# Kernel optimization log

Measured on AMD Instinct MI355X. Metric: run time of the kernel, lower is better.

Reference implementation:

```python
import jax, jax.numpy as jnp
import numpy as np
from jax import lax

WIN = 11
SIGMA = 1.5
C1 = 0.01 ** 2
C2 = 0.03 ** 2


def _gauss_window(c):
    x = np.arange(WIN) - WIN // 2
    g = np.exp(-(x ** 2) / (2.0 * SIGMA ** 2))
    g = g / g.sum()
    w2d = np.outer(g, g).astype(np.float32)  # [11,11]
    return jnp.asarray(np.broadcast_to(w2d, (c, 1, WIN, WIN)).copy())


def _dwconv(x, kernel, groups):
    # x: [B,C,H,W], kernel: [C,1,kh,kw] depthwise, stride 1, SAME padding
    return lax.conv_general_dilated(
        x, kernel, window_strides=(1, 1), padding='SAME',
        dimension_numbers=('NCHW', 'OIHW', 'NCHW'),
        feature_group_count=groups)


_SOBEL_X = jnp.asarray(np.array([[-1, 0, 1], [-2, 0, 2], [-1, 0, 1]], np.float32))
_SOBEL_Y = jnp.asarray(np.array([[1, 2, 1], [0, 0, 0], [-1, -2, -1]], np.float32))


def _sobel_xy(x):
    # x: [B,3,H,W] -> depthwise 3x3 sobel on each channel (same as per-channel conv2d)
    c = x.shape[1]
    kx = jnp.broadcast_to(_SOBEL_X, (c, 1, 3, 3))
    ky = jnp.broadcast_to(_SOBEL_Y, (c, 1, 3, 3))
    return _dwconv(x, kx, c), _dwconv(x, ky, c)


def _rgb2ycrcb(im):
    R, G, B = im[:, 0:1], im[:, 1:2], im[:, 2:3]
    Y = 0.299 * R + 0.587 * G + 0.114 * B
    Cr = (R - Y) * 0.713 + 0.5
    Cb = (B - Y) * 0.564 + 0.5
    return Y, Cr, Cb


def _ssim(img1, img2, channel):
    w = _gauss_window(channel)
    mu1 = _dwconv(img1, w, channel)
    mu2 = _dwconv(img2, w, channel)
    mu1_sq = mu1 * mu1
    mu2_sq = mu2 * mu2
    mu12 = mu1 * mu2
    s1 = _dwconv(img1 * img1, w, channel) - mu1_sq
    s2 = _dwconv(img2 * img2, w, channel) - mu2_sq
    s12 = _dwconv(img1 * img2, w, channel) - mu12
    ssim_map = ((2 * mu12 + C1) * (2 * s12 + C2)) / ((mu1_sq + mu2_sq + C1) * (s1 + s2 + C2))
    return ssim_map.mean()


def _l1(a, b):
    return jnp.mean(jnp.abs(a - b))


def setup_inputs() -> dict:
    key = jax.random.key(0)
    k1, k2, k3 = jax.random.split(key, 3)
    shp = (16, 3, 512, 512)
    return {
        'input_vis': jax.random.uniform(k1, shp, jnp.float32),
        'input_ir': jax.random.uniform(k2, shp, jnp.float32),
        'fuse': jax.random.uniform(k3, shp, jnp.float32),
    }


def reference(input_vis, input_ir, fuse):
    # color components
    _, Cr_F, Cb_F = _rgb2ycrcb(fuse)
    _, Cr_V, Cb_V = _rgb2ycrcb(input_vis)
    Y_ir = input_ir[:, 0:1]

    # sobel gradients (depthwise over 3 channels == per-channel conv + cat)
    Fgx, Fgy = _sobel_xy(fuse)
    Vgx, Vgy = _sobel_xy(input_vis)
    Igx, Igy = _sobel_xy(input_ir)
    joint_gx = jnp.maximum(Vgx, Igx)
    joint_gy = jnp.maximum(Vgy, Igy)
    joint_int = jnp.maximum(input_vis, input_ir)

    con_loss = _l1(fuse, joint_int)
    gradient_loss = 0.5 * _l1(Fgx, joint_gx) + 0.5 * _l1(Fgy, joint_gy)
    color_loss = _l1(Cb_F, Cb_V) + _l1(Cr_F, Cr_V)

    # SSIM: rgb-vs-fused (3ch) and ir-Y vs gray(fused) (1ch)
    ssim_rgb = _ssim(input_vis, fuse, 3)
    gray_fused = (0.2989 * fuse[:, 0:1] + 0.587 * fuse[:, 1:2] + 0.114 * fuse[:, 2:3])
    ssim_ir = _ssim(Y_ir, gray_fused, 1)
    ssim_loss = 1.0 - (ssim_rgb + ssim_ir) / 2.0

    return 0.5 * con_loss + 0.2 * gradient_loss + 1.0 * color_loss + 0.1 * ssim_loss
```

## Files before the change

kernel.cpp:

```cpp
#include <hip/hip_runtime.h>

#define IMG_H 512
#define IMG_W 512
#define CH_STRIDE (IMG_H*IMG_W)
#define IMG_STRIDE (3*CH_STRIDE)

using f4 = __attribute__((ext_vector_type(4))) float;
using h2 = __attribute__((ext_vector_type(2))) _Float16;
using h4 = __attribute__((ext_vector_type(4))) _Float16;
using h8 = __attribute__((ext_vector_type(8))) _Float16;

#define NSLOT 64
#define SLOT_F 32

__global__ __launch_bounds__(256) void k_zero(float* __restrict__ acc) {
  int i = threadIdx.x;
  *(f4*)&acc[i*8]     = f4{0,0,0,0};
  *(f4*)&acc[i*8 + 4] = f4{0,0,0,0};
}

__device__ __forceinline__ float block_sum(float v, float* red) {
  #pragma unroll
  for (int o = 32; o > 0; o >>= 1) v += __shfl_down(v, o, 64);
  __syncthreads();
  if ((threadIdx.x & 63) == 0) red[threadIdx.x >> 6] = v;
  __syncthreads();
  return red[0] + red[1] + red[2] + red[3];
}

__device__ __forceinline__ h8 splat8(_Float16 v) { return h8{v,v,v,v,v,v,v,v}; }

#define R1W 68
#define R1N (18*R1W)

#define SXW 80
#define SXH 26
#define HB8 264
#define SSIM_SX_B (SXH*SXW*2)
#define SSIM_HB_B (SXH*HB8*2)
#define SMEM_BYTES (2*SSIM_SX_B + SSIM_HB_B)

#define N_SSIM 16384

__global__ __launch_bounds__(256, 7) void k_main(
    const float* __restrict__ vis, const float* __restrict__ ir,
    const float* __restrict__ fuse, float* __restrict__ acc)
{
  __shared__ __align__(16) char smem[SMEM_BYTES];
  __shared__ float red[4];
  const int tid = threadIdx.x;
  const int bid = blockIdx.x;
  float* aslot = acc + (bid & (NSLOT-1))*SLOT_F;

  if (bid < N_SSIM) {
    const int z = bid >> 8;
    const int n = z >> 2, pair = z & 3;
    const int x0 = (bid & 7)*64;
    const int y0 = ((bid >> 3) & 31)*16;
    _Float16* sx = (_Float16*)smem;
    _Float16* sy = (_Float16*)(smem + SSIM_SX_B);
    _Float16* hb = (_Float16*)(smem + 2*SSIM_SX_B);

    _Float16 gh[11];
    h2 gh2[11];
    {
      const float gu[6] = {0.00386592014f, 0.02856550078f, 0.13533528324f,
                           0.41111229050f, 0.80073740292f, 1.0f};
      float g[11], gs = 0.f;
      #pragma unroll
      for (int i = 0; i < 11; ++i) { g[i] = gu[i < 6 ? i : 10 - i]; gs += g[i]; }
      #pragma unroll
      for (int i = 0; i < 11; ++i) {
        g[i] /= gs;
        gh[i] = (_Float16)g[i];
        gh2[i] = h2{gh[i], gh[i]};
      }
    }

    if (pair < 3) {
      const float* xb = vis  + (n*3 + pair)*CH_STRIDE;
      const float* yb = fuse + (n*3 + pair)*CH_STRIDE;
      for (int i = tid; i < SXH*20; i += 256) {
        int row = i / 20, k = i - row*20;
        int gy = y0 - 5 + row, gx = x0 - 8 + 4*k;
        f4 xv = {0,0,0,0}, yv = {0,0,0,0};
        if ((unsigned)gy < IMG_H && (unsigned)gx < IMG_W) {
          int off = gy*IMG_W + gx;
          xv = *(const f4*)&xb[off];
          yv = *(const f4*)&yb[off];
        }
        int ib = row*SXW + 4*k;
        *(h4*)&sx[ib] = h4{(_Float16)xv.x,(_Float16)xv.y,(_Float16)xv.z,(_Float16)xv.w};
        *(h4*)&sy[ib] = h4{(_Float16)yv.x,(_Float16)yv.y,(_Float16)yv.z,(_Float16)yv.w};
      }
    } else {
      const float* xb = ir   + n*IMG_STRIDE;
      const float* fb = fuse + n*IMG_STRIDE;
      for (int i = tid; i < SXH*20; i += 256) {
        int row = i / 20, k = i - row*20;
        int gy = y0 - 5 + row, gx = x0 - 8 + 4*k;
        f4 xv = {0,0,0,0}, yv = {0,0,0,0};
        if ((unsigned)gy < IMG_H && (unsigned)gx < IMG_W) {
          int off = gy*IMG_W + gx;
          xv = *(const f4*)&xb[off];
          f4 rr = *(const f4*)&fb[off];
          f4 gg = *(const f4*)&fb[off + CH_STRIDE];
          f4 bb = *(const f4*)&fb[off + 2*CH_STRIDE];
          #pragma unroll
          for (int j = 0; j < 4; ++j)
            yv[j] = 0.2989f*rr[j] + 0.587f*gg[j] + 0.114f*bb[j];
        }
        int ib = row*SXW + 4*k;
        *(h4*)&sx[ib] = h4{(_Float16)xv.x,(_Float16)xv.y,(_Float16)xv.z,(_Float16)xv.w};
        *(h4*)&sy[ib] = h4{(_Float16)yv.x,(_Float16)yv.y,(_Float16)yv.z,(_Float16)yv.w};
      }
    }
    __syncthreads();

    for (int t = tid; t < SXH*8; t += 256) {
      int row = t >> 3, p0 = (t & 7)*4;
      int base = row*SXW + p0*2;
      h8 xa0 = *(const h8*)&sx[base];
      h8 xa1 = *(const h8*)&sx[base+8];
      h8 xa2 = *(const h8*)&sx[base+16];
      h8 yb0 = *(const h8*)&sy[base];
      h8 yb1 = *(const h8*)&sy[base+8];
      h8 yb2 = *(const h8*)&sy[base+16];
      _Float16 wa[21], wb[21];
      #pragma unroll
      for (int u = 0; u < 21; ++u) {
        wa[u] = (u < 8 ? xa0[u] : (u < 16 ? xa1[u-8] : xa2[u-16]));
        wb[u] = (u < 8 ? yb0[u] : (u < 16 ? yb1[u-8] : yb2[u-16]));
      }
      h2 pa[14], pb[14], pp[14], pq[14];
      #pragma unroll
      for (int u = 0; u < 14; ++u) {
        pa[u] = h2{wa[u+3], wa[u+7]};
        pb[u] = h2{wb[u+3], wb[u+7]};
        pp[u] = pa[u]*pa[u] + pb[u]*pb[u];
        pq[u] = pa[u]*pb[u];
      }
      h2 cA[4], cB[4], cP[4], cQ[4];
      #pragma unroll
      for (int j = 0; j < 4; ++j) { cA[j]=h2{0,0}; cB[j]=h2{0,0}; cP[j]=h2{0,0}; cQ[j]=h2{0,0}; }
      #pragma unroll
      for (int k = 0; k < 11; ++k) {
        h2 gk = gh2[k];
        #pragma unroll
        for (int j = 0; j < 4; ++j) {
          cA[j] += gk * pa[k+j];
          cB[j] += gk * pb[k+j];
          cP[j] += gk * pp[k+j];
          cQ[j] += gk * pq[k+j];
        }
      }
      #pragma unroll
      for (int p = 0; p < 4; ++p) {
        int j0 = 2*p, j1 = 2*p + 1;
        _Float16 a0 = (j0 < 4) ? cA[j0][0] : cA[j0-4][1];
        _Float16 b0 = (j0 < 4) ? cB[j0][0] : cB[j0-4][1];
        _Float16 P0 = (j0 < 4) ? cP[j0][0] : cP[j0-4][1];
        _Float16 q0 = (j0 < 4) ? cQ[j0][0] : cQ[j0-4][1];
        _Float16 a1 = (j1 < 4) ? cA[j1][0] : cA[j1-4][1];
        _Float16 b1 = (j1 < 4) ? cB[j1][0] : cB[j1-4][1];
        _Float16 P1 = (j1 < 4) ? cP[j1][0] : cP[j1-4][1];
        _Float16 q1 = (j1 < 4) ? cQ[j1][0] : cQ[j1-4][1];
        *(h8*)&hb[row*HB8 + (p0 + p)*8] = h8{a0,b0,P0,q0,a1,b1,P1,q1};
      }
    }
    __syncthreads();

    const int xp = tid & 31;
    const int ybase = (tid >> 5)*2;
    h8 vacc[2];
    #pragma unroll
    for (int m = 0; m < 2; ++m) vacc[m] = splat8((_Float16)0.f);
    #pragma unroll
    for (int r = 0; r < 12; ++r) {
      h8 rv = *(const h8*)&hb[(ybase + r)*HB8 + xp*8];
      #pragma unroll
      for (int m = 0; m < 2; ++m) {
        int k = r - m;
        if (k >= 0 && k < 11) vacc[m] += splat8(gh[k]) * rv;
      }
    }

    float ss = 0.f;
    #pragma unroll
    for (int m = 0; m < 2; ++m) {
      #pragma unroll
      for (int px = 0; px < 2; ++px) {
        float mu1 = (float)vacc[m][4*px + 0];
        float mu2 = (float)vacc[m][4*px + 1];
        float sP  = (float)vacc[m][4*px + 2];
        float sQ  = (float)vacc[m][4*px + 3];
        float mu12 = mu1*mu2, mss = mu1*mu1 + mu2*mu2;
        float s12 = sQ - mu12, sps = sP - mss;
        ss += ((2.f*mu12 + 1e-4f)*(2.f*s12 + 9e-4f)) /
              ((mss + 1e-4f)*(sps + 9e-4f));
      }
    }
    float tot = block_sum(ss, red);
    if (tid == 0) atomicAdd(&aslot[(pair == 3) ? 6 : 5], tot);

  } else {
    const int r = bid - N_SSIM;
    const int x0 = (r & 7)*64;
    const int y0 = ((r >> 3) & 31)*16;
    const int n  = r >> 8;
    float* s = (float*)smem;
    const int ox = (tid & 15)*4;
    const int oy = tid >> 4;

    float con=0.f, gxs=0.f, gys=0.f, cbs=0.f, crs=0.f;
    float pv[3][4], pf[3][4];

    for (int c = 0; c < 3; ++c) {
      const float* pv0 = vis  + (n*3 + c)*CH_STRIDE;
      const float* pi0 = ir   + (n*3 + c)*CH_STRIDE;
      const float* pf0 = fuse + (n*3 + c)*CH_STRIDE;
      for (int i = tid; i < 864; i += 256) {
        int f = i / 288;
        int rr = i - f*288;
        int row = rr >> 4, k = rr & 15;
        int gy = y0 - 1 + row, gx = x0 + 4*k;
        f4 v = {0,0,0,0};
        const float* bp = (f == 0) ? pv0 : ((f == 1) ? pi0 : pf0);
        if ((unsigned)gy < IMG_H) v = *(const f4*)&bp[gy*IMG_W + gx];
        float* dst = s + f*R1N + row*R1W + 1 + 4*k;
        dst[0]=v.x; dst[1]=v.y; dst[2]=v.z; dst[3]=v.w;
      }
      if (tid < 108) {
        int f = tid / 36;
        int rr = tid - f*36;
        int row = rr >> 1, side = rr & 1;
        int gy = y0 - 1 + row;
        int gx = side ? (x0 + 64) : (x0 - 1);
        float v = 0.f;
        const float* bp = (f == 0) ? pv0 : ((f == 1) ? pi0 : pf0);
        if ((unsigned)gx < IMG_W && (unsigned)gy < IMG_H) v = bp[gy*IMG_W + gx];
        s[f*R1N + row*R1W + (side ? 65 : 0)] = v;
      }
      __syncthreads();

      float cen[3][4], gxv[3][4], gyv[3][4];
      #pragma unroll
      for (int t = 0; t < 3; ++t) {
        const float* sf = s + t*R1N;
        float r0[8], r1[8], r2[8];
        {
          f4 a = *(const f4*)&sf[(oy+0)*R1W + ox], b = *(const f4*)&sf[(oy+0)*R1W + ox + 4];
          r0[0]=a.x; r0[1]=a.y; r0[2]=a.z; r0[3]=a.w; r0[4]=b.x; r0[5]=b.y; r0[6]=b.z; r0[7]=b.w;
        }
        {
          f4 a = *(const f4*)&sf[(oy+1)*R1W + ox], b = *(const f4*)&sf[(oy+1)*R1W + ox + 4];
          r1[0]=a.x; r1[1]=a.y; r1[2]=a.z; r1[3]=a.w; r1[4]=b.x; r1[5]=b.y; r1[6]=b.z; r1[7]=b.w;
        }
        {
          f4 a = *(const f4*)&sf[(oy+2)*R1W + ox], b = *(const f4*)&sf[(oy+2)*R1W + ox + 4];
          r2[0]=a.x; r2[1]=a.y; r2[2]=a.z; r2[3]=a.w; r2[4]=b.x; r2[5]=b.y; r2[6]=b.z; r2[7]=b.w;
        }
        #pragma unroll
        for (int j = 0; j < 4; ++j) {
          gxv[t][j] = (r0[j+2]-r0[j]) + 2.f*(r1[j+2]-r1[j]) + (r2[j+2]-r2[j]);
          gyv[t][j] = (r0[j] + 2.f*r0[j+1] + r0[j+2]) - (r2[j] + 2.f*r2[j+1] + r2[j+2]);
          cen[t][j] = r1[j+1];
        }
      }
      #pragma unroll
      for (int j = 0; j < 4; ++j) {
        con += fabsf(cen[2][j] - fmaxf(cen[0][j], cen[1][j]));
        gxs += fabsf(gxv[2][j] - fmaxf(gxv[0][j], gxv[1][j]));
        gys += fabsf(gyv[2][j] - fmaxf(gyv[0][j], gyv[1][j]));
        pv[c][j] = cen[0][j];
        pf[c][j] = cen[2][j];
      }
      __syncthreads();
    }

    #pragma unroll
    for (int j = 0; j < 4; ++j) {
      float Yf = 0.299f*pf[0][j] + 0.587f*pf[1][j] + 0.114f*pf[2][j];
      float Yv = 0.299f*pv[0][j] + 0.587f*pv[1][j] + 0.114f*pv[2][j];
      crs += fabsf(0.713f*((pf[0][j]-Yf) - (pv[0][j]-Yv)));
      cbs += fabsf(0.564f*((pf[2][j]-Yf) - (pv[2][j]-Yv)));
    }

    float r0 = block_sum(con, red);
    float r1 = block_sum(gxs, red);
    float r2 = block_sum(gys, red);
    float r3 = block_sum(cbs, red);
    float r4 = block_sum(crs, red);
    if (tid == 0) {
      atomicAdd(&aslot[0], r0);
      atomicAdd(&aslot[1], r1);
      atomicAdd(&aslot[2], r2);
      atomicAdd(&aslot[3], r3);
      atomicAdd(&aslot[4], r4);
    }
  }
}

__global__ __launch_bounds__(64) void k_final(
    const float* __restrict__ acc, float* __restrict__ out)
{
  int lane = threadIdx.x;
  float s[7];
  #pragma unroll
  for (int c = 0; c < 7; ++c) {
    float x = acc[lane*SLOT_F + c];
    #pragma unroll
    for (int o = 32; o > 0; o >>= 1) x += __shfl_down(x, o, 64);
    s[c] = x;
  }
  if (lane == 0) {
    const float N3 = 16.f*3.f*512.f*512.f;
    const float N1 = 16.f*512.f*512.f;
    float con_loss  = s[0] / N3;
    float grad_loss = 0.5f*(s[1]/N3) + 0.5f*(s[2]/N3);
    float color_loss = s[3]/N1 + s[4]/N1;
    float ssim_loss = 1.f - (s[5]/N3 + s[6]/N1)*0.5f;
    out[0] = 0.5f*con_loss + 0.2f*grad_loss + color_loss + 0.1f*ssim_loss;
  }
}

extern "C" void kernel_launch(void* const* d_in, const int* in_sizes, int n_in,
                              void* d_out, int out_size, void* d_ws, size_t ws_size,
                              hipStream_t stream) {
  (void)in_sizes; (void)n_in; (void)out_size; (void)ws_size;
  const float* vis  = (const float*)d_in[0];
  const float* ir   = (const float*)d_in[1];
  const float* fuse = (const float*)d_in[2];
  float* out = (float*)d_out;
  float* acc = (float*)d_ws;

  k_zero<<<dim3(1,1,1), dim3(256,1,1), 0, stream>>>(acc);
  k_main<<<dim3(20480,1,1), dim3(256,1,1), 0, stream>>>(vis, ir, fuse, acc);
  k_final<<<dim3(1,1,1), dim3(64,1,1), 0, stream>>>(acc, out);
}
```

Before: 256.0 us.

## Compute SSIM separable Gaussian blurs with MFMA matrix instructions

Replaces the packed-half VALU horizontal and vertical 11-tap Gaussian passes with MFMA 16x16x32 f16 matrix multiplies against banded Toeplitz weight matrices built in shared memory. The squared and product terms (x²+y², xy) are now formed in fp32 at load time and stored as four fp16 planes. The intermediate buffer uses an XOR swizzle to avoid LDS bank conflicts. Shared memory grows and the occupancy hint drops from 7 to 4 blocks per CU, which trades latency hiding for matrix-core throughput.

```diff
diff --git a/kernel.cpp b/kernel.cpp
--- a/kernel.cpp
+++ b/kernel.cpp
@@ -5,10 +5,10 @@
 #define CH_STRIDE (IMG_H*IMG_W)
 #define IMG_STRIDE (3*CH_STRIDE)
 
-using f4 = __attribute__((ext_vector_type(4))) float;
-using h2 = __attribute__((ext_vector_type(2))) _Float16;
-using h4 = __attribute__((ext_vector_type(4))) _Float16;
-using h8 = __attribute__((ext_vector_type(8))) _Float16;
+using f4    = __attribute__((ext_vector_type(4))) float;
+using h4    = __attribute__((ext_vector_type(4))) _Float16;
+using h8    = __attribute__((ext_vector_type(8))) _Float16;
+using f32x4 = __attribute__((ext_vector_type(4))) float;
 
 #define NSLOT 64
 #define SLOT_F 32
@@ -28,21 +28,22 @@
   return red[0] + red[1] + red[2] + red[3];
 }
 
-__device__ __forceinline__ h8 splat8(_Float16 v) { return h8{v,v,v,v,v,v,v,v}; }
-
 #define R1W 68
 #define R1N (18*R1W)
 
-#define SXW 80
+#define SXW 88
 #define SXH 26
-#define HB8 264
-#define SSIM_SX_B (SXH*SXW*2)
-#define SSIM_HB_B (SXH*HB8*2)
-#define SMEM_BYTES (2*SSIM_SX_B + SSIM_HB_B)
+#define SF_STRIDE (SXH*SXW)
+#define HB_OFF    (4*SF_STRIDE)
+#define HB_F      (64*32)
+#define WH_OFF    (HB_OFF + 4*HB_F)
+#define WV_OFF    (WH_OFF + 512)
+#define SMEM_H    (WV_OFF + 512)
+#define SMEM_BYTES (SMEM_H*2)
 
 #define N_SSIM 16384
 
-__global__ __launch_bounds__(256, 7) void k_main(
+__global__ __launch_bounds__(256, 4) void k_main(
     const float* __restrict__ vis, const float* __restrict__ ir,
     const float* __restrict__ fuse, float* __restrict__ acc)
 {
@@ -57,24 +58,18 @@
     const int n = z >> 2, pair = z & 3;
     const int x0 = (bid & 7)*64;
     const int y0 = ((bid >> 3) & 31)*16;
-    _Float16* sx = (_Float16*)smem;
-    _Float16* sy = (_Float16*)(smem + SSIM_SX_B);
-    _Float16* hb = (_Float16*)(smem + 2*SSIM_SX_B);
-
-    _Float16 gh[11];
-    h2 gh2[11];
-    {
-      const float gu[6] = {0.00386592014f, 0.02856550078f, 0.13533528324f,
-                           0.41111229050f, 0.80073740292f, 1.0f};
-      float g[11], gs = 0.f;
-      #pragma unroll
-      for (int i = 0; i < 11; ++i) { g[i] = gu[i < 6 ? i : 10 - i]; gs += g[i]; }
-      #pragma unroll
-      for (int i = 0; i < 11; ++i) {
-        g[i] /= gs;
-        gh[i] = (_Float16)g[i];
-        gh2[i] = h2{gh[i], gh[i]};
-      }
+    _Float16* S = (_Float16*)smem;
+
+    for (int i = tid; i < 1024; i += 256) {
+      int m = i & 511;
+      int col = m >> 5, k = m & 31;
+      int j = (i < 512) ? (k - col - 3) : (k - col);
+      float w = 0.f;
+      if ((unsigned)j < 11u) {
+        float d = (float)(j - 5);
+        w = exp2f(-d*d*0.32059889798f) * 0.26601255681f;
+      }
+      S[(i < 512 ? WH_OFF : WV_OFF) + m] = (_Float16)w;
     }
 
     if (pair < 3) {
@@ -90,8 +85,19 @@
           yv = *(const f4*)&yb[off];
         }
         int ib = row*SXW + 4*k;
-        *(h4*)&sx[ib] = h4{(_Float16)xv.x,(_Float16)xv.y,(_Float16)xv.z,(_Float16)xv.w};
-        *(h4*)&sy[ib] = h4{(_Float16)yv.x,(_Float16)yv.y,(_Float16)yv.z,(_Float16)yv.w};
+        h4 ax, by, pp, qq;
+        #pragma unroll
+        for (int j = 0; j < 4; ++j) {
+          float xa = xv[j], ya = yv[j];
+          ax[j] = (_Float16)xa;
+          by[j] = (_Float16)ya;
+          pp[j] = (_Float16)(xa*xa + ya*ya);
+          qq[j] = (_Float16)(xa*ya);
+        }
+        *(h4*)&S[0*SF_STRIDE + ib] = ax;
+        *(h4*)&S[1*SF_STRIDE + ib] = by;
+        *(h4*)&S[2*SF_STRIDE + ib] = pp;
+        *(h4*)&S[3*SF_STRIDE + ib] = qq;
       }
     } else {
       const float* xb = ir   + n*IMG_STRIDE;
@@ -111,89 +117,73 @@
             yv[j] = 0.2989f*rr[j] + 0.587f*gg[j] + 0.114f*bb[j];
         }
         int ib = row*SXW + 4*k;
-        *(h4*)&sx[ib] = h4{(_Float16)xv.x,(_Float16)xv.y,(_Float16)xv.z,(_Float16)xv.w};
-        *(h4*)&sy[ib] = h4{(_Float16)yv.x,(_Float16)yv.y,(_Float16)yv.z,(_Float16)yv.w};
-      }
-    }
-    __syncthreads();
-
-    for (int t = tid; t < SXH*8; t += 256) {
-      int row = t >> 3, p0 = (t & 7)*4;
-      int base = row*SXW + p0*2;
-      h8 xa0 = *(const h8*)&sx[base];
-      h8 xa1 = *(const h8*)&sx[base+8];
-      h8 xa2 = *(const h8*)&sx[base+16];
-      h8 yb0 = *(const h8*)&sy[base];
-      h8 yb1 = *(const h8*)&sy[base+8];
-      h8 yb2 = *(const h8*)&sy[base+16];
-      _Float16 wa[21], wb[21];
-      #pragma unroll
-      for (int u = 0; u < 21; ++u) {
-        wa[u] = (u < 8 ? xa0[u] : (u < 16 ? xa1[u-8] : xa2[u-16]));
-        wb[u] = (u < 8 ? yb0[u] : (u < 16 ? yb1[u-8] : yb2[u-16]));
-      }
-      h2 pa[14], pb[14], pp[14], pq[14];
-      #pragma unroll
-      for (int u = 0; u < 14; ++u) {
-        pa[u] = h2{wa[u+3], wa[u+7]};
-        pb[u] = h2{wb[u+3], wb[u+7]};
-        pp[u] = pa[u]*pa[u] + pb[u]*pb[u];
-        pq[u] = pa[u]*pb[u];
-      }
-      h2 cA[4], cB[4], cP[4], cQ[4];
-      #pragma unroll
-      for (int j = 0; j < 4; ++j) { cA[j]=h2{0,0}; cB[j]=h2{0,0}; cP[j]=h2{0,0}; cQ[j]=h2{0,0}; }
-      #pragma unroll
-      for (int k = 0; k < 11; ++k) {
-        h2 gk = gh2[k];
+        h4 ax, by, pp, qq;
         #pragma unroll
         for (int j = 0; j < 4; ++j) {
-          cA[j] += gk * pa[k+j];
-          cB[j] += gk * pb[k+j];
-          cP[j] += gk * pp[k+j];
-          cQ[j] += gk * pq[k+j];
-        }
-      }
-      #pragma unroll
-      for (int p = 0; p < 4; ++p) {
-        int j0 = 2*p, j1 = 2*p + 1;
-        _Float16 a0 = (j0 < 4) ? cA[j0][0] : cA[j0-4][1];
-        _Float16 b0 = (j0 < 4) ? cB[j0][0] : cB[j0-4][1];
-        _Float16 P0 = (j0 < 4) ? cP[j0][0] : cP[j0-4][1];
-        _Float16 q0 = (j0 < 4) ? cQ[j0][0] : cQ[j0-4][1];
-        _Float16 a1 = (j1 < 4) ? cA[j1][0] : cA[j1-4][1];
-        _Float16 b1 = (j1 < 4) ? cB[j1][0] : cB[j1-4][1];
-        _Float16 P1 = (j1 < 4) ? cP[j1][0] : cP[j1-4][1];
-        _Float16 q1 = (j1 < 4) ? cQ[j1][0] : cQ[j1-4][1];
-        *(h8*)&hb[row*HB8 + (p0 + p)*8] = h8{a0,b0,P0,q0,a1,b1,P1,q1};
+          float xa = xv[j], ya = yv[j];
+          ax[j] = (_Float16)xa;
+          by[j] = (_Float16)ya;
+          pp[j] = (_Float16)(xa*xa + ya*ya);
+          qq[j] = (_Float16)(xa*ya);
+        }
+        *(h4*)&S[0*SF_STRIDE + ib] = ax;
+        *(h4*)&S[1*SF_STRIDE + ib] = by;
+        *(h4*)&S[2*SF_STRIDE + ib] = pp;
+        *(h4*)&S[3*SF_STRIDE + ib] = qq;
       }
     }
     __syncthreads();
 
-    const int xp = tid & 31;
-    const int ybase = (tid >> 5)*2;
-    h8 vacc[2];
-    #pragma unroll
-    for (int m = 0; m < 2; ++m) vacc[m] = splat8((_Float16)0.f);
-    #pragma unroll
-    for (int r = 0; r < 12; ++r) {
-      h8 rv = *(const h8*)&hb[(ybase + r)*HB8 + xp*8];
-      #pragma unroll
-      for (int m = 0; m < 2; ++m) {
-        int k = r - m;
-        if (k >= 0 && k < 11) vacc[m] += splat8(gh[k]) * rv;
-      }
-    }
+    const int lr = tid & 15;
+    const int lg = (tid >> 4) & 3;
+    const int wv = tid >> 6;
+
+    {
+      h8 bh = *(const h8*)&S[WH_OFF + lr*32 + lg*8];
+      const int xo = wv*16;
+      #pragma unroll
+      for (int rt = 0; rt < 2; ++rt) {
+        int row_s = rt*16 + lr;
+        int rcl = row_s > 25 ? 25 : row_s;
+        bool zz = row_s > 25;
+        #pragma unroll
+        for (int f = 0; f < 4; ++f) {
+          h8 a = *(const h8*)&S[f*SF_STRIDE + rcl*SXW + xo + lg*8];
+          if (zz) a = h8{(_Float16)0,(_Float16)0,(_Float16)0,(_Float16)0,
+                         (_Float16)0,(_Float16)0,(_Float16)0,(_Float16)0};
+          f32x4 d = __builtin_amdgcn_mfma_f32_16x16x32_f16(
+                        a, bh, f32x4{0.f,0.f,0.f,0.f}, 0, 0, 0);
+          int px = xo + lr;
+          int k0 = rt*16 + lg*4;
+          h4 hv;
+          #pragma unroll
+          for (int r = 0; r < 4; ++r) hv[r] = (_Float16)d[r];
+          int sgrp = (px ^ (px >> 2)) & 3;
+          int b = k0 << 1;
+          int sb = ((((b >> 4) ^ sgrp) << 4) | (b & 15));
+          *(h4*)&S[HB_OFF + f*HB_F + px*32 + (sb >> 1)] = hv;
+        }
+      }
+    }
+    __syncthreads();
 
     float ss = 0.f;
-    #pragma unroll
-    for (int m = 0; m < 2; ++m) {
-      #pragma unroll
-      for (int px = 0; px < 2; ++px) {
-        float mu1 = (float)vacc[m][4*px + 0];
-        float mu2 = (float)vacc[m][4*px + 1];
-        float sP  = (float)vacc[m][4*px + 2];
-        float sQ  = (float)vacc[m][4*px + 3];
+    {
+      h8 bv = *(const h8*)&S[WV_OFF + lr*32 + lg*8];
+      const int pxA = wv*16 + lr;
+      const int sgrp = (pxA ^ (pxA >> 2)) & 3;
+      f32x4 dd[4];
+      #pragma unroll
+      for (int f = 0; f < 4; ++f) {
+        int gi = lg ^ sgrp;
+        h8 a = *(const h8*)&S[HB_OFF + f*HB_F + pxA*32 + gi*8];
+        dd[f] = __builtin_amdgcn_mfma_f32_16x16x32_f16(
+                    a, bv, f32x4{0.f,0.f,0.f,0.f}, 0, 0, 0);
+      }
+      #pragma unroll
+      for (int r = 0; r < 4; ++r) {
+        float mu1 = dd[0][r], mu2 = dd[1][r];
+        float sP  = dd[2][r], sQ  = dd[3][r];
         float mu12 = mu1*mu2, mss = mu1*mu1 + mu2*mu2;
         float s12 = sQ - mu12, sps = sP - mss;
         ss += ((2.f*mu12 + 1e-4f)*(2.f*s12 + 9e-4f)) /
```

Measured after the change: 253.6 us. No clear change (-0.9%).
